# Optimization experiments

Hardware: AMD Instinct MI355X
Metric: run time of the kernel (lower is better)

The kernel has to match this reference:

```python
import jax, jax.numpy as jnp
import numpy as np

# Dimensions
T = 1024      # tokens
D = 1024      # d_model
DFF = 1024    # expert intermediate dim
R = 64        # tucker rank (r_in == r_out)
G = 8         # n_group
E = 32        # experts_per_group
NEXP = G * E  # 256 routed experts
K = 8         # top-k


def setup_inputs() -> dict:
    key = jax.random.key(0)
    ks = jax.random.split(key, 12)
    s = 0.02
    return {
        "x": jax.random.normal(ks[0], (T, D), jnp.float32),
        "Wg": jax.random.normal(ks[1], (D, NEXP), jnp.float32) * s,
        "uin_gate": jax.random.normal(ks[2], (G, D, R), jnp.float32) * s,
        "core_gate": jax.random.normal(ks[3], (G, E, R, R), jnp.float32) * s,
        "uout_gate": jax.random.normal(ks[4], (G, R, DFF), jnp.float32) * s,
        "uin_up": jax.random.normal(ks[5], (G, D, R), jnp.float32) * s,
        "core_up": jax.random.normal(ks[6], (G, E, R, R), jnp.float32) * s,
        "uout_up": jax.random.normal(ks[7], (G, R, DFF), jnp.float32) * s,
        "uin_down": jax.random.normal(ks[8], (G, DFF, R), jnp.float32) * s,
        "core_down": jax.random.normal(ks[9], (G, E, R, R), jnp.float32) * s,
        "uout_down": jax.random.normal(ks[10], (G, R, D), jnp.float32) * s,
    }


def _moe_forward(x, Wg, uin_gate, core_gate, uout_gate,
                 uin_up, core_up, uout_up,
                 uin_down, core_down, uout_down):
    Tn, d = x.shape
    # Router: top-k over 256 experts, softmax over the k logits (fp32 as in torch)
    logits = x @ Wg                                   # [T, NEXP]
    w, sel = jax.lax.top_k(logits, K)                 # [T, K]
    w = jax.nn.softmax(w.astype(jnp.float32), axis=-1).astype(x.dtype)

    e = sel.reshape(-1)                               # [F] global expert id
    g = e // E                                        # [F] group id
    tok = jnp.repeat(jnp.arange(Tn), K)               # [F] source token id
    mask = (g[:, None] == jnp.arange(G)[None, :]).astype(x.dtype)  # [F, G]

    def gather_in(uin):
        # project tokens with every group's u_in once, then gather per pair
        pre = jnp.einsum('td,gdr->gtr', x, uin)       # [G, T, R]
        return pre[g, tok]                            # [F, R]

    def core_apply(xin, core):
        # per-pair Tucker core slice bmm: x.unsqueeze(1) @ core[rel_idx]
        slices = core.reshape(G * E, R, R)[e]         # [F, R, R] gather
        return jnp.einsum('fr,fro->fo', xin, slices)  # [F, R]

    def group_out(h, U):
        # per-pair group-specific projection: h[f] @ U[g_f]
        out = jnp.zeros((h.shape[0], U.shape[-1]), h.dtype)
        for gi in range(G):  # fixed small loop over 8 groups
            out = out + (h * mask[:, gi:gi + 1]) @ U[gi]
        return out

    gate_h = group_out(core_apply(gather_in(uin_gate), core_gate), uout_gate)  # [F, DFF]
    up_h = group_out(core_apply(gather_in(uin_up), core_up), uout_up)          # [F, DFF]
    act = jax.nn.silu(gate_h) * up_h                                           # SwiGLU
    xin_d = group_out(act, uin_down)                                           # [F, R]
    out_f = group_out(core_apply(xin_d, core_down), uout_down)                 # [F, D]
    out_f = out_f * w.reshape(-1)[:, None]
    # scatter-add expert outputs back to tokens
    return jax.ops.segment_sum(out_f, tok, num_segments=Tn)


def reference(x, Wg, uin_gate, core_gate, uout_gate,
              uin_up, core_up, uout_up,
              uin_down, core_down, uout_down):
    return _moe_forward(x, Wg, uin_gate, core_gate, uout_gate,
                        uin_up, core_up, uout_up,
                        uin_down, core_down, uout_down)
```

## Files before the change

### kernel.cpp

```cpp
#include <hip/hip_runtime.h>
#include <hip/hip_bf16.h>
#include <math.h>


#define T_ 1024
#define D_ 1024
#define DFF_ 1024
#define R_ 64
#define G_ 8
#define E_ 32
#define NEXP_ 256
#define K_ 8
#define F_ 8192
#define LKZ_ 8
#define LTB_ 8
#define PKZ_ 2
#define DKZ_ 4
#define LP_ 72

typedef short bf16x8 __attribute__((ext_vector_type(8)));
typedef float f32x4 __attribute__((ext_vector_type(4)));

__device__ __forceinline__ unsigned short f2bf(float f) {
  unsigned int u = __float_as_uint(f);
  u += 0x7fffu + ((u >> 16) & 1u);
  return (unsigned short)(u >> 16);
}

__device__ __forceinline__ void stage_tile(short* dst, const unsigned short* src,
                                           int gp, int tid) {
  for (int idx = tid; idx < 512; idx += 256) {
    int r = idx >> 3, c8 = (idx & 7) << 3;
    *(uint4*)&dst[r * LP_ + c8] = *(const uint4*)&src[(size_t)r * gp + c8];
  }
}

__device__ __forceinline__ void stage_tile_guard(short* dst, const unsigned short* src,
                                                 int gp, int rows_valid, int tid) {
  for (int idx = tid; idx < 512; idx += 256) {
    int r = idx >> 3, c8 = (idx & 7) << 3;
    uint4 v = make_uint4(0u, 0u, 0u, 0u);
    if (r < rows_valid) v = *(const uint4*)&src[(size_t)r * gp + c8];
    *(uint4*)&dst[r * LP_ + c8] = v;
  }
}

__device__ __forceinline__ void mma_strip(const short* As, const short* Bs,
                                          int ms, int lane, f32x4* acc) {
  int lm = lane & 15;
  int lk = (lane >> 4) << 3;
#pragma unroll
  for (int kc = 0; kc < 64; kc += 32) {
    bf16x8 a = *(const bf16x8*)&As[(ms + lm) * LP_ + kc + lk];
#pragma unroll
    for (int nt = 0; nt < 4; ++nt) {
      bf16x8 b = *(const bf16x8*)&Bs[(nt * 16 + lm) * LP_ + kc + lk];
      acc[nt] = __builtin_amdgcn_mfma_f32_16x16x32_bf16(a, b, acc[nt], 0, 0, 0);
    }
  }
}

__global__ __launch_bounds__(256) void k_prep_logits(
    const float* __restrict__ x, const float* __restrict__ Wg,
    const float* __restrict__ s0, const float* __restrict__ s1,
    const float* __restrict__ s2, const float* __restrict__ s3,
    const float* __restrict__ s4, const float* __restrict__ s5,
    unsigned short* __restrict__ xb,
    unsigned short* __restrict__ d0, unsigned short* __restrict__ d1,
    unsigned short* __restrict__ d2, unsigned short* __restrict__ d3,
    unsigned short* __restrict__ d4, unsigned short* __restrict__ d5,
    int* __restrict__ cnt, float* __restrict__ lp) {
  __shared__ float shbuf[64 * 65];
  int b = blockIdx.x;
  if (b < 896) {
    int id = b >> 7, rem = b & 127, g = rem >> 4, tile = rem & 15;
    if (id == 6) {
      size_t base = ((size_t)g * 16 + tile) * 8192;
      for (int i = threadIdx.x; i < 2048; i += 256) {
        size_t idx = base + (size_t)i * 4;
        float4 v = *(const float4*)&x[idx];
        xb[idx + 0] = f2bf(v.x);
        xb[idx + 1] = f2bf(v.y);
        xb[idx + 2] = f2bf(v.z);
        xb[idx + 3] = f2bf(v.w);
      }
      if (g == 0 && tile == 0) cnt[threadIdx.x] = 0;
      return;
    }
    const float* src = id == 0 ? s0 : id == 1 ? s1 : id == 2 ? s2 : id == 3 ? s3 : id == 4 ? s4 : s5;
    unsigned short* dst = id == 0 ? d0 : id == 1 ? d1 : id == 2 ? d2 : id == 3 ? d3 : id == 4 ? d4 : d5;
    if (id < 3) {
      int r0 = tile * 64;
      for (int idx = threadIdx.x; idx < 4096; idx += 256) {
        int r = idx >> 6, c = idx & 63;
        shbuf[r * 65 + c] = src[((size_t)g * 1024 + r0 + r) * 64 + c];
      }
      __syncthreads();
      for (int idx = threadIdx.x; idx < 4096; idx += 256) {
        int c = idx >> 6, r = idx & 63;
        dst[((size_t)g * 64 + c) * 1024 + r0 + r] = f2bf(shbuf[r * 65 + c]);
      }
    } else {
      int c0 = tile * 64;
      for (int idx = threadIdx.x; idx < 4096; idx += 256) {
        int r = idx >> 6, c = idx & 63;
        shbuf[r * 65 + c] = src[((size_t)g * 64 + r) * 1024 + c0 + c];
      }
      __syncthreads();
      if (id == 5) {
        for (int idx = threadIdx.x; idx < 4096; idx += 256) {
          int c = idx >> 6, r = idx & 63;
          dst[(size_t)(c0 + c) * 512 + g * 64 + r] = f2bf(shbuf[r * 65 + c]);
        }
      } else {
        for (int idx = threadIdx.x; idx < 4096; idx += 256) {
          int c = idx >> 6, r = idx & 63;
          dst[((size_t)g * 1024 + c0 + c) * 64 + r] = f2bf(shbuf[r * 65 + c]);
        }
      }
    }
    return;
  }
  int lb = b - 896;
  int t0 = (lb & 127) * LTB_;
  int z = lb >> 7;
  int e = threadIdx.x;
  float* xs = shbuf;
  float a[LTB_] = {};
  int dc = z * 128;
  {
    int idx = threadIdx.x * 4;
    int tl = idx >> 7, d = idx & 127;
    *(float4*)&xs[tl * 128 + d] = *(const float4*)&x[(size_t)(t0 + tl) * D_ + dc + d];
  }
  __syncthreads();
#pragma unroll 8
  for (int d2 = 0; d2 < 128; ++d2) {
    float wv = Wg[(size_t)(dc + d2) * NEXP_ + e];
#pragma unroll
    for (int j = 0; j < LTB_; ++j) a[j] = fmaf(xs[j * 128 + d2], wv, a[j]);
  }
  size_t base = (size_t)z * T_ * NEXP_;
#pragma unroll
  for (int j = 0; j < LTB_; ++j)
    lp[base + (size_t)(t0 + j) * NEXP_ + e] = a[j];
}

__global__ __launch_bounds__(256) void k_pre_topk(
    const unsigned short* __restrict__ xb,
    const unsigned short* __restrict__ uinT_g, const unsigned short* __restrict__ uinT_u,
    const float* __restrict__ lp,
    float* __restrict__ Pgp, float* __restrict__ Pup,
    int* __restrict__ sel, float* __restrict__ wsm,
    int* __restrict__ rank, int* __restrict__ cnt) {
  __shared__ short sh2[2 * 64 * LP_];
  int b = blockIdx.x;
  if (b < 512) {
    int tile = b & 15, g = (b >> 4) & 7, zz = b >> 7;
    int gu = zz >> 1, kz = zz & 1;
    const unsigned short* U = gu ? uinT_u : uinT_g;
    float* P = gu ? Pup : Pgp;
    int t0 = tile * 64;
    short* As = sh2;
    short* Bs = sh2 + 64 * LP_;
    int tid = threadIdx.x, lane = tid & 63, ms = (tid >> 6) * 16;
    f32x4 acc[4] = {};
    int dlo = kz * (D_ / PKZ_);
    for (int dc = dlo; dc < dlo + D_ / PKZ_; dc += 64) {
      stage_tile(As, xb + (size_t)t0 * D_ + dc, D_, tid);
      stage_tile(Bs, U + (size_t)g * 64 * 1024 + dc, 1024, tid);
      __syncthreads();
      mma_strip(As, Bs, ms, lane, acc);
      __syncthreads();
    }
    int lm = lane & 15, lq = (lane >> 4) * 4;
#pragma unroll
    for (int nt = 0; nt < 4; ++nt)
#pragma unroll
      for (int r = 0; r < 4; ++r)
        P[((size_t)(kz * G_ + g) * T_ + t0 + ms + lq + r) * R_ + nt * 16 + lm] = acc[nt][r];
    return;
  }
  int tb = b - 512;
  int wave = threadIdx.x >> 6;
  int lane = threadIdx.x & 63;
  int t = tb * 4 + wave;
  float v[4];
  int idx[4];
#pragma unroll
  for (int j = 0; j < 4; ++j) {
    idx[j] = lane + 64 * j;
    float s = 0.f;
#pragma unroll
    for (int z = 0; z < LKZ_; ++z)
      s += lp[(size_t)z * T_ * NEXP_ + (size_t)t * NEXP_ + idx[j]];
    v[j] = s;
  }
  float topv[K_];
  int topi[K_];
#pragma unroll
  for (int k = 0; k < K_; ++k) {
    float bv = v[0];
    int bi = idx[0];
#pragma unroll
    for (int j = 1; j < 4; ++j)
      if (v[j] > bv || (v[j] == bv && idx[j] < bi)) { bv = v[j]; bi = idx[j]; }
#pragma unroll
    for (int off = 32; off > 0; off >>= 1) {
      float ov = __shfl_xor(bv, off);
      int oi = __shfl_xor(bi, off);
      if (ov > bv || (ov == bv && oi < bi)) { bv = ov; bi = oi; }
    }
    topv[k] = bv;
    topi[k] = bi;
#pragma unroll
    for (int j = 0; j < 4; ++j)
      if (idx[j] == bi) v[j] = -INFINITY;
  }
  float m = topv[0];
  float ev[K_];
  float s = 0.f;
#pragma unroll
  for (int k = 0; k < K_; ++k) { ev[k] = expf(topv[k] - m); s += ev[k]; }
  float inv = 1.f / s;
  if (lane < K_) {
    sel[t * K_ + lane] = topi[lane];
    wsm[t * K_ + lane] = ev[lane] * inv;
    rank[t * K_ + lane] = atomicAdd(&cnt[topi[lane]], 1);
  }
}

__global__ __launch_bounds__(256) void k_scan(const int* __restrict__ cnt,
                                              int* __restrict__ off) {
  __shared__ int s[NEXP_];
  int i = threadIdx.x;
  s[i] = cnt[i];
  __syncthreads();
  for (int d = 1; d < NEXP_; d <<= 1) {
    int v = (i >= d) ? s[i - d] : 0;
    __syncthreads();
    s[i] += v;
    __syncthreads();
  }
  off[i + 1] = s[i];
  if (i == 0) off[0] = 0;
}

__global__ __launch_bounds__(256) void k_core_gu(const float* __restrict__ Pgp,
                                                 const float* __restrict__ Pup,
                                                 const float* __restrict__ core_g,
                                                 const float* __restrict__ core_u,
                                                 const int* __restrict__ sel,
                                                 const int* __restrict__ rank,
                                                 const int* __restrict__ off,
                                                 unsigned short* __restrict__ xgb,
                                                 unsigned short* __restrict__ xub) {
  int pl = threadIdx.x >> 6;
  int o = threadIdx.x & 63;
  int f = blockIdx.x * 4 + pl;
  int t = f >> 3;
  int e = sel[f];
  int g = e >> 5;
  int p = off[e] + rank[f];
  __shared__ float rg[4][64], ru[4][64];
  float sg = 0.f, su = 0.f;
#pragma unroll
  for (int kz = 0; kz < PKZ_; ++kz) {
    sg += Pgp[((size_t)(kz * G_ + g) * T_ + t) * R_ + o];
    su += Pup[((size_t)(kz * G_ + g) * T_ + t) * R_ + o];
  }
  rg[pl][o] = sg;
  ru[pl][o] = su;
  __syncthreads();
  const float* cg = core_g + (size_t)e * R_ * R_;
  const float* cu = core_u + (size_t)e * R_ * R_;
  float ag = 0.f, au = 0.f;
#pragma unroll 8
  for (int r = 0; r < R_; ++r) {
    ag = fmaf(rg[pl][r], cg[r * R_ + o], ag);
    au = fmaf(ru[pl][r], cu[r * R_ + o], au);
  }
  xgb[(size_t)p * R_ + o] = f2bf(ag);
  xub[(size_t)p * R_ + o] = f2bf(au);
}

__global__ __launch_bounds__(256) void k_fused_ad(const unsigned short* __restrict__ xgb,
                                                  const unsigned short* __restrict__ xub,
                                                  const unsigned short* __restrict__ uoutT_g,
                                                  const unsigned short* __restrict__ uoutT_u,
                                                  const unsigned short* __restrict__ uinT_d,
                                                  const int* __restrict__ off,
                                                  float* __restrict__ xdp) {
  int g = blockIdx.y;
  int kz = blockIdx.z;
  int p0 = off[g * E_];
  int pend = off[g * E_ + E_];
  int ntiles = (pend - p0 + 63) >> 6;
  __shared__ short Ag[64 * LP_], Au[64 * LP_];
  __shared__ short Bg[64 * LP_], Bu[64 * LP_], Bd[64 * LP_];
  __shared__ short Pt[64 * LP_];
  int tid = threadIdx.x, lane = tid & 63, ms = (tid >> 6) * 16;
  int lm = lane & 15, lq = (lane >> 4) * 4;
  for (int tile = blockIdx.x; tile < ntiles; tile += gridDim.x) {
    int pbase = p0 + tile * 64;
    int rv = pend - pbase; if (rv > 64) rv = 64;
    stage_tile_guard(Ag, xgb + (size_t)pbase * R_, R_, rv, tid);
    stage_tile_guard(Au, xub + (size_t)pbase * R_, R_, rv, tid);
    f32x4 accd[4] = {};
#pragma unroll
    for (int c4 = 0; c4 < 4; ++c4) {
      int cc = kz * (DFF_ / DKZ_) + c4 * 64;
      stage_tile(Bg, uoutT_g + ((size_t)g * DFF_ + cc) * R_, R_, tid);
      stage_tile(Bu, uoutT_u + ((size_t)g * DFF_ + cc) * R_, R_, tid);
      stage_tile(Bd, uinT_d + (size_t)g * 64 * 1024 + cc, 1024, tid);
      __syncthreads();
      f32x4 accg[4] = {}, accu[4] = {};
      mma_strip(Ag, Bg, ms, lane, accg);
      mma_strip(Au, Bu, ms, lane, accu);
#pragma unroll
      for (int nt = 0; nt < 4; ++nt)
#pragma unroll
        for (int r = 0; r < 4; ++r) {
          float gv = accg[nt][r];
          float av = gv / (1.f + expf(-gv)) * accu[nt][r];
          Pt[(ms + lq + r) * LP_ + nt * 16 + lm] = (short)f2bf(av);
        }
      mma_strip(Pt, Bd, ms, lane, accd);
      __syncthreads();
    }
#pragma unroll
    for (int nt = 0; nt < 4; ++nt)
#pragma unroll
      for (int r = 0; r < 4; ++r) {
        int p = pbase + ms + lq + r;
        if (p < pend) xdp[((size_t)kz * F_ + p) * R_ + nt * 16 + lm] = accd[nt][r];
      }
    __syncthreads();
  }
}

__global__ __launch_bounds__(256) void k_down_accY(const float* __restrict__ xdp,
                                                   const float* __restrict__ core_d,
                                                   const int* __restrict__ sel,
                                                   const int* __restrict__ rank,
                                                   const float* __restrict__ wsm,
                                                   const int* __restrict__ off,
                                                   unsigned short* __restrict__ Ybf) {
  int t = blockIdx.x;
  int w = threadIdx.x >> 6, o = threadIdx.x & 63;
  __shared__ float xs[4][64];
  __shared__ float yl[4][G_][64];
  float y[G_] = {};
#pragma unroll
  for (int kk = 0; kk < 2; ++kk) {
    int f = t * K_ + w * 2 + kk;
    int e = sel[f];
    int g = e >> 5;
    int p = off[e] + rank[f];
    float s = 0.f;
#pragma unroll
    for (int kz = 0; kz < DKZ_; ++kz) s += xdp[((size_t)kz * F_ + p) * R_ + o];
    __syncthreads();
    xs[w][o] = s;
    __syncthreads();
    const float* cd = core_d + (size_t)e * R_ * R_;
    float a = 0.f;
#pragma unroll 8
    for (int r = 0; r < R_; ++r) a = fmaf(xs[w][r], cd[r * R_ + o], a);
    y[g] += wsm[f] * a;
  }
#pragma unroll
  for (int g = 0; g < G_; ++g) yl[w][g][o] = y[g];
  __syncthreads();
  for (int idx = threadIdx.x; idx < 512; idx += 256) {
    int g = idx >> 6, oo = idx & 63;
    float v = yl[0][g][oo] + yl[1][g][oo] + yl[2][g][oo] + yl[3][g][oo];
    Ybf[(size_t)t * 512 + g * 64 + oo] = f2bf(v);
  }
}

__global__ __launch_bounds__(256) void k_fin(const unsigned short* __restrict__ Ybf,
                                             const unsigned short* __restrict__ Uod2T,
                                             float* __restrict__ out) {
  int t0 = blockIdx.x * 64;
  int d0 = blockIdx.y * 64;
  __shared__ short As[64 * LP_], Bs[64 * LP_];
  __shared__ float Os[64 * 68];
  int tid = threadIdx.x, lane = tid & 63, ms = (tid >> 6) * 16;
  int lm = lane & 15, lq = (lane >> 4) * 4;
  f32x4 acc[4] = {};
  for (int kc = 0; kc < 512; kc += 64) {
    stage_tile(As, Ybf + (size_t)t0 * 512 + kc, 512, tid);
    stage_tile(Bs, Uod2T + (size_t)d0 * 512 + kc, 512, tid);
    __syncthreads();
    mma_strip(As, Bs, ms, lane, acc);
    __syncthreads();
  }
#pragma unroll
  for (int nt = 0; nt < 4; ++nt)
#pragma unroll
    for (int r = 0; r < 4; ++r)
      Os[(ms + lq + r) * 68 + nt * 16 + lm] = acc[nt][r];
  __syncthreads();
  for (int idx = tid; idx < 1024; idx += 256) {
    int r = idx >> 4, c4 = (idx & 15) << 2;
    *(float4*)&out[(size_t)(t0 + r) * D_ + d0 + c4] = *(const float4*)&Os[r * 68 + c4];
  }
}

extern "C" void kernel_launch(void* const* d_in, const int* in_sizes, int n_in,
                              void* d_out, int out_size, void* d_ws, size_t ws_size,
                              hipStream_t stream) {
  const float* x = (const float*)d_in[0];
  const float* Wg = (const float*)d_in[1];
  const float* uin_gate = (const float*)d_in[2];
  const float* core_gate = (const float*)d_in[3];
  const float* uout_gate = (const float*)d_in[4];
  const float* uin_up = (const float*)d_in[5];
  const float* core_up = (const float*)d_in[6];
  const float* uout_up = (const float*)d_in[7];
  const float* uin_down = (const float*)d_in[8];
  const float* core_down = (const float*)d_in[9];
  const float* uout_down = (const float*)d_in[10];
  float* out = (float*)d_out;

  char* ws = (char*)d_ws;
  size_t o = 0;
  auto alloc = [&](size_t bytes) { size_t r = o; o = (o + bytes + 255) & ~(size_t)255; return r; };
  size_t o_lp = alloc((size_t)LKZ_ * T_ * NEXP_ * 4);
  size_t o_sel = alloc(F_ * 4);
  size_t o_wsm = alloc(F_ * 4);
  size_t o_rank = alloc(F_ * 4);
  size_t o_cnt = alloc(NEXP_ * 4);
  size_t o_off = alloc((NEXP_ + 1) * 4);
  size_t o_xb = alloc((size_t)T_ * D_ * 2);
  size_t o_uinT_g = alloc((size_t)G_ * 64 * 1024 * 2);
  size_t o_uinT_u = alloc((size_t)G_ * 64 * 1024 * 2);
  size_t o_uinT_d = alloc((size_t)G_ * 64 * 1024 * 2);
  size_t o_uoutT_g = alloc((size_t)G_ * 1024 * 64 * 2);
  size_t o_uoutT_u = alloc((size_t)G_ * 1024 * 64 * 2);
  size_t o_Uod2T = alloc((size_t)D_ * 512 * 2);
  size_t o_xgb = alloc((size_t)F_ * R_ * 2);
  size_t o_xub = alloc((size_t)F_ * R_ * 2);
  size_t o_Y = alloc((size_t)T_ * 512 * 2);
  size_t o_pgp = alloc((size_t)PKZ_ * G_ * T_ * R_ * 4);
  size_t o_pup = alloc((size_t)PKZ_ * G_ * T_ * R_ * 4);
  size_t o_xdp = alloc((size_t)DKZ_ * F_ * R_ * 4);
  (void)ws_size;

  float* lp = (float*)(ws + o_lp);
  int* sel = (int*)(ws + o_sel);
  float* wsm = (float*)(ws + o_wsm);
  int* rank = (int*)(ws + o_rank);
  int* cnt = (int*)(ws + o_cnt);
  int* off = (int*)(ws + o_off);
  unsigned short* xb = (unsigned short*)(ws + o_xb);
  unsigned short* uinT_g = (unsigned short*)(ws + o_uinT_g);
  unsigned short* uinT_u = (unsigned short*)(ws + o_uinT_u);
  unsigned short* uinT_d = (unsigned short*)(ws + o_uinT_d);
  unsigned short* uoutT_g = (unsigned short*)(ws + o_uoutT_g);
  unsigned short* uoutT_u = (unsigned short*)(ws + o_uoutT_u);
  unsigned short* Uod2T = (unsigned short*)(ws + o_Uod2T);
  unsigned short* xgb = (unsigned short*)(ws + o_xgb);
  unsigned short* xub = (unsigned short*)(ws + o_xub);
  unsigned short* Ybf = (unsigned short*)(ws + o_Y);
  float* pgp = (float*)(ws + o_pgp);
  float* pup = (float*)(ws + o_pup);
  float* xdp = (float*)(ws + o_xdp);

  k_prep_logits<<<1920, 256, 0, stream>>>(x, Wg, uin_gate, uin_up, uin_down,
                                          uout_gate, uout_up, uout_down, xb,
                                          uinT_g, uinT_u, uinT_d,
                                          uoutT_g, uoutT_u, Uod2T, cnt, lp);
  k_pre_topk<<<768, 256, 0, stream>>>(xb, uinT_g, uinT_u, lp, pgp, pup, sel, wsm, rank, cnt);
  k_scan<<<1, 256, 0, stream>>>(cnt, off);
  k_core_gu<<<F_ / 4, 256, 0, stream>>>(pgp, pup, core_gate, core_up, sel, rank, off, xgb, xub);
  k_fused_ad<<<dim3(16, G_, DKZ_), 256, 0, stream>>>(xgb, xub, uoutT_g, uoutT_u, uinT_d, off, xdp);
  k_down_accY<<<T_, 256, 0, stream>>>(xdp, core_down, sel, rank, wsm, off, Ybf);
  k_fin<<<dim3(16, 16), 256, 0, stream>>>(Ybf, Uod2T, out);
}
```

Baseline: 204.1 us.

## Reorganize core-slice kernels per expert with shared-memory cores and inverse index

The scan kernel now also builds an inverse permutation (sorted position to pair id) and a forward map (pair id to sorted position). With these, the gate/up core kernel and the down core kernel run one block per expert half and stage that expert's 64x64 core in shared memory once, instead of re-reading the core slice from global memory for every pair. The down path is split into a per-expert core apply that writes weighted results to a new buffer and a separate per-token group accumulation kernel. The router logit loop also reads four Wg rows at once and loads x as float4. In exchange there is one more launch, an extra fp32 workspace buffer, serial scatter work inside the single-block scan, and per-expert load imbalance.

```diff
diff --git a/kernel.cpp b/kernel.cpp
--- a/kernel.cpp
+++ b/kernel.cpp
@@ -134,11 +134,22 @@
     *(float4*)&xs[tl * 128 + d] = *(const float4*)&x[(size_t)(t0 + tl) * D_ + dc + d];
   }
   __syncthreads();
-#pragma unroll 8
-  for (int d2 = 0; d2 < 128; ++d2) {
-    float wv = Wg[(size_t)(dc + d2) * NEXP_ + e];
-#pragma unroll
-    for (int j = 0; j < LTB_; ++j) a[j] = fmaf(xs[j * 128 + d2], wv, a[j]);
+#pragma unroll 2
+  for (int d2 = 0; d2 < 128; d2 += 4) {
+    float w0 = Wg[(size_t)(dc + d2 + 0) * NEXP_ + e];
+    float w1 = Wg[(size_t)(dc + d2 + 1) * NEXP_ + e];
+    float w2 = Wg[(size_t)(dc + d2 + 2) * NEXP_ + e];
+    float w3 = Wg[(size_t)(dc + d2 + 3) * NEXP_ + e];
+#pragma unroll
+    for (int j = 0; j < LTB_; ++j) {
+      float4 xv = *(const float4*)&xs[j * 128 + d2];
+      float aj = a[j];
+      aj = fmaf(xv.x, w0, aj);
+      aj = fmaf(xv.y, w1, aj);
+      aj = fmaf(xv.z, w2, aj);
+      aj = fmaf(xv.w, w3, aj);
+      a[j] = aj;
+    }
   }
   size_t base = (size_t)z * T_ * NEXP_;
 #pragma unroll
@@ -231,10 +242,16 @@
 }
 
 __global__ __launch_bounds__(256) void k_scan(const int* __restrict__ cnt,
-                                              int* __restrict__ off) {
+                                              int* __restrict__ off,
+                                              const int* __restrict__ sel,
+                                              const int* __restrict__ rank,
+                                              int* __restrict__ ipos,
+                                              int* __restrict__ pf) {
   __shared__ int s[NEXP_];
+  __shared__ int ex[NEXP_];
   int i = threadIdx.x;
-  s[i] = cnt[i];
+  int c0 = cnt[i];
+  s[i] = c0;
   __syncthreads();
   for (int d = 1; d < NEXP_; d <<= 1) {
     int v = (i >= d) ? s[i - d] : 0;
@@ -242,46 +259,69 @@
     s[i] += v;
     __syncthreads();
   }
+  ex[i] = s[i] - c0;
   off[i + 1] = s[i];
   if (i == 0) off[0] = 0;
+  __syncthreads();
+#pragma unroll 4
+  for (int f = i; f < F_; f += 256) {
+    int p = ex[sel[f]] + rank[f];
+    ipos[p] = f;
+    pf[f] = p;
+  }
 }
 
 __global__ __launch_bounds__(256) void k_core_gu(const float* __restrict__ Pgp,
                                                  const float* __restrict__ Pup,
                                                  const float* __restrict__ core_g,
                                                  const float* __restrict__ core_u,
-                                                 const int* __restrict__ sel,
-                                                 const int* __restrict__ rank,
+                                                 const int* __restrict__ ipos,
                                                  const int* __restrict__ off,
                                                  unsigned short* __restrict__ xgb,
                                                  unsigned short* __restrict__ xub) {
-  int pl = threadIdx.x >> 6;
-  int o = threadIdx.x & 63;
-  int f = blockIdx.x * 4 + pl;
-  int t = f >> 3;
-  int e = sel[f];
+  int e = blockIdx.x >> 1, half = blockIdx.x & 1;
   int g = e >> 5;
-  int p = off[e] + rank[f];
+  __shared__ float cg[64 * 64], cu[64 * 64];
   __shared__ float rg[4][64], ru[4][64];
-  float sg = 0.f, su = 0.f;
-#pragma unroll
-  for (int kz = 0; kz < PKZ_; ++kz) {
-    sg += Pgp[((size_t)(kz * G_ + g) * T_ + t) * R_ + o];
-    su += Pup[((size_t)(kz * G_ + g) * T_ + t) * R_ + o];
-  }
-  rg[pl][o] = sg;
-  ru[pl][o] = su;
+  int tid = threadIdx.x;
+  for (int i = tid; i < 4096; i += 256) {
+    cg[i] = core_g[(size_t)e * 4096 + i];
+    cu[i] = core_u[(size_t)e * 4096 + i];
+  }
+  int p0 = off[e], n = off[e + 1] - p0;
+  int hn = (n + 1) >> 1;
+  int i0 = half * hn;
+  int i1 = i0 + hn; if (i1 > n) i1 = n;
+  int pl = tid >> 6, o = tid & 63;
   __syncthreads();
-  const float* cg = core_g + (size_t)e * R_ * R_;
-  const float* cu = core_u + (size_t)e * R_ * R_;
-  float ag = 0.f, au = 0.f;
+  for (int ib = i0; ib < i1; ib += 4) {
+    int i = ib + pl;
+    bool valid = i < i1;
+    int p = p0 + i;
+    float sg = 0.f, su = 0.f;
+    if (valid) {
+      int t = ipos[p] >> 3;
+#pragma unroll
+      for (int kz = 0; kz < PKZ_; ++kz) {
+        sg += Pgp[((size_t)(kz * G_ + g) * T_ + t) * R_ + o];
+        su += Pup[((size_t)(kz * G_ + g) * T_ + t) * R_ + o];
+      }
+    }
+    __syncthreads();
+    rg[pl][o] = sg;
+    ru[pl][o] = su;
+    __syncthreads();
+    if (valid) {
+      float ag = 0.f, au = 0.f;
 #pragma unroll 8
-  for (int r = 0; r < R_; ++r) {
-    ag = fmaf(rg[pl][r], cg[r * R_ + o], ag);
-    au = fmaf(ru[pl][r], cu[r * R_ + o], au);
-  }
-  xgb[(size_t)p * R_ + o] = f2bf(ag);
-  xub[(size_t)p * R_ + o] = f2bf(au);
+      for (int r = 0; r < R_; ++r) {
+        ag = fmaf(rg[pl][r], cg[r * R_ + o], ag);
+        au = fmaf(ru[pl][r], cu[r * R_ + o], au);
+      }
+      xgb[(size_t)p * R_ + o] = f2bf(ag);
+      xub[(size_t)p * R_ + o] = f2bf(au);
+    }
+  }
 }
 
 __global__ __launch_bounds__(256) void k_fused_ad(const unsigned short* __restrict__ xgb,
@@ -339,44 +379,63 @@
   }
 }
 
-__global__ __launch_bounds__(256) void k_down_accY(const float* __restrict__ xdp,
+__global__ __launch_bounds__(256) void k_down_core(const float* __restrict__ xdp,
                                                    const float* __restrict__ core_d,
-                                                   const int* __restrict__ sel,
-                                                   const int* __restrict__ rank,
+                                                   const int* __restrict__ ipos,
                                                    const float* __restrict__ wsm,
                                                    const int* __restrict__ off,
-                                                   unsigned short* __restrict__ Ybf) {
-  int t = blockIdx.x;
-  int w = threadIdx.x >> 6, o = threadIdx.x & 63;
+                                                   float* __restrict__ zd) {
+  int e = blockIdx.x >> 1, half = blockIdx.x & 1;
+  __shared__ float cd[64 * 64];
   __shared__ float xs[4][64];
-  __shared__ float yl[4][G_][64];
+  int tid = threadIdx.x;
+  for (int i = tid; i < 4096; i += 256) cd[i] = core_d[(size_t)e * 4096 + i];
+  int p0 = off[e], n = off[e + 1] - p0;
+  int hn = (n + 1) >> 1;
+  int i0 = half * hn;
+  int i1 = i0 + hn; if (i1 > n) i1 = n;
+  int pl = tid >> 6, o = tid & 63;
+  __syncthreads();
+  for (int ib = i0; ib < i1; ib += 4) {
+    int i = ib + pl;
+    bool valid = i < i1;
+    int p = p0 + i;
+    float s = 0.f, w = 0.f;
+    if (valid) {
+#pragma unroll
+      for (int kz = 0; kz < DKZ_; ++kz) s += xdp[((size_t)kz * F_ + p) * R_ + o];
+      w = wsm[ipos[p]];
+    }
+    __syncthreads();
+    xs[pl][o] = s;
+    __syncthreads();
+    if (valid) {
+      float a = 0.f;
+#pragma unroll 8
+      for (int r = 0; r < R_; ++r) a = fmaf(xs[pl][r], cd[r * R_ + o], a);
+      zd[(size_t)p * R_ + o] = w * a;
+    }
+  }
+}
+
+__global__ __launch_bounds__(256) void k_accY(const float* __restrict__ zd,
+                                              const int* __restrict__ sel,
+                                              const int* __restrict__ pf,
+                                              unsigned short* __restrict__ Ybf) {
+  int t = blockIdx.x * 4 + (threadIdx.x >> 6);
+  int o = threadIdx.x & 63;
   float y[G_] = {};
 #pragma unroll
-  for (int kk = 0; kk < 2; ++kk) {
-    int f = t * K_ + w * 2 + kk;
-    int e = sel[f];
-    int g = e >> 5;
-    int p = off[e] + rank[f];
-    float s = 0.f;
-#pragma unroll
-    for (int kz = 0; kz < DKZ_; ++kz) s += xdp[((size_t)kz * F_ + p) * R_ + o];
-    __syncthreads();
-    xs[w][o] = s;
-    __syncthreads();
-    const float* cd = core_d + (size_t)e * R_ * R_;
-    float a = 0.f;
-#pragma unroll 8
-    for (int r = 0; r < R_; ++r) a = fmaf(xs[w][r], cd[r * R_ + o], a);
-    y[g] += wsm[f] * a;
-  }
-#pragma unroll
-  for (int g = 0; g < G_; ++g) yl[w][g][o] = y[g];
-  __syncthreads();
-  for (int idx = threadIdx.x; idx < 512; idx += 256) {
-    int g = idx >> 6, oo = idx & 63;
-    float v = yl[0][g][oo] + yl[1][g][oo] + yl[2][g][oo] + yl[3][g][oo];
-    Ybf[(size_t)t * 512 + g * 64 + oo] = f2bf(v);
-  }
+  for (int k = 0; k < K_; ++k) {
+    int f = t * K_ + k;
+    int g = sel[f] >> 5;
+    float v = zd[(size_t)pf[f] * R_ + o];
+#pragma unroll
+    for (int gi = 0; gi < G_; ++gi) y[gi] += (g == gi) ? v : 0.f;
+  }
+#pragma unroll
+  for (int gi = 0; gi < G_; ++gi)
+    Ybf[(size_t)t * 512 + gi * 64 + o] = f2bf(y[gi]);
 }
 
 __global__ __launch_bounds__(256) void k_fin(const unsigned short* __restrict__ Ybf,
@@ -431,6 +490,8 @@
   size_t o_sel = alloc(F_ * 4);
   size_t o_wsm = alloc(F_ * 4);
   size_t o_rank = alloc(F_ * 4);
+  size_t o_ipos = alloc(F_ * 4);
+  size_t o_pf = alloc(F_ * 4);
   size_t o_cnt = alloc(NEXP_ * 4);
   size_t o_off = alloc((NEXP_ + 1) * 4);
   size_t o_xb = alloc((size_t)T_ * D_ * 2);
@@ -446,12 +507,15 @@
   size_t o_pgp = alloc((size_t)PKZ_ * G_ * T_ * R_ * 4);
   size_t o_pup = alloc((size_t)PKZ_ * G_ * T_ * R_ * 4);
   size_t o_xdp = alloc((size_t)DKZ_ * F_ * R_ * 4);
+  size_t o_zd = alloc((size_t)F_ * R_ * 4);
   (void)ws_size;
 
   float* lp = (float*)(ws + o_lp);
   int* sel = (int*)(ws + o_sel);
   float* wsm = (float*)(ws + o_wsm);
   int* rank = (int*)(ws + o_rank);
+  int* ipos = (int*)(ws + o_ipos);
+  int* pf = (int*)(ws + o_pf);
   int* cnt = (int*)(ws + o_cnt);
   int* off = (int*)(ws + o_off);
   unsigned short* xb = (unsigned short*)(ws + o_xb);
@@ -467,15 +531,17 @@
   float* pgp = (float*)(ws + o_pgp);
   float* pup = (float*)(ws + o_pup);
   float* xdp = (float*)(ws + o_xdp);
+  float* zd = (float*)(ws + o_zd);
 
   k_prep_logits<<<1920, 256, 0, stream>>>(x, Wg, uin_gate, uin_up, uin_down,
                                           uout_gate, uout_up, uout_down, xb,
                                           uinT_g, uinT_u, uinT_d,
                                           uoutT_g, uoutT_u, Uod2T, cnt, lp);
   k_pre_topk<<<768, 256, 0, stream>>>(xb, uinT_g, uinT_u, lp, pgp, pup, sel, wsm, rank, cnt);
-  k_scan<<<1, 256, 0, stream>>>(cnt, off);
-  k_core_gu<<<F_ / 4, 256, 0, stream>>>(pgp, pup, core_gate, core_up, sel, rank, off, xgb, xub);
+  k_scan<<<1, 256, 0, stream>>>(cnt, off, sel, rank, ipos, pf);
+  k_core_gu<<<NEXP_ * 2, 256, 0, stream>>>(pgp, pup, core_gate, core_up, ipos, off, xgb, xub);
   k_fused_ad<<<dim3(16, G_, DKZ_), 256, 0, stream>>>(xgb, xub, uoutT_g, uoutT_u, uinT_d, off, xdp);
-  k_down_accY<<<T_, 256, 0, stream>>>(xdp, core_down, sel, rank, wsm, off, Ybf);
+  k_down_core<<<NEXP_ * 2, 256, 0, stream>>>(xdp, core_down, ipos, wsm, off, zd);
+  k_accY<<<T_ / 4, 256, 0, stream>>>(zd, sel, pf, Ybf);
   k_fin<<<dim3(16, 16), 256, 0, stream>>>(Ybf, Uod2T, out);
 }
```

Result: slower. 212.2 us (+3.9%).
